# Optimization experiments

Hardware: AMD Instinct MI355X
Metric: run time of the kernel (lower is better)

## Reference

```python
import jax, jax.numpy as jnp
import numpy as np

IN_FEATURES = 8192
OUT_FEATURES = 8192
BATCH = 1024


def setup_inputs() -> dict:
    key = jax.random.key(0)
    kx, kw, kb = jax.random.split(key, 3)
    bound = 1.0 / np.sqrt(IN_FEATURES)  # nn.Linear default init range
    x = jax.random.normal(kx, (BATCH, IN_FEATURES), dtype=jnp.float32)
    W = jax.random.uniform(kw, (OUT_FEATURES, IN_FEATURES), minval=-bound, maxval=bound, dtype=jnp.float32)
    b = jax.random.uniform(kb, (OUT_FEATURES,), minval=-bound, maxval=bound, dtype=jnp.float32)
    return {"x": x, "W": W, "b": b}


def reference(x, W, b):
    # Linear: (B, I) @ (I, O) + (O,) -> (B, O)
    y = jnp.einsum('bi,oi->bo', x, W) + b
    # sum over dim=1, keepdim -> (B, 1)
    y = jnp.sum(y, axis=1, keepdims=True)
    # max over size-1 dim (keepdim) -> identity
    y = jnp.max(y, axis=1, keepdims=True)
    # mean over size-1 dim -> identity
    y = jnp.mean(y, axis=1, keepdims=True)
    # logsumexp over size-1 dim (twice) -> identity
    y = jax.nn.logsumexp(y, axis=1, keepdims=True)
    y = jax.nn.logsumexp(y, axis=1, keepdims=True)
    return y
```

## Files before the change

kernel.cpp:

```cpp
#include <hip/hip_runtime.h>

#define I_FEAT 8192
#define O_FEAT 8192
#define BATCH  1024

#define NS        256
#define ROWS_PB   32
#define CCHUNKS   4
#define SGROUPS   8

using f4 = __attribute__((ext_vector_type(4))) float;

__global__ __launch_bounds__(256) void colsum_partial_kernel(
    const float* __restrict__ W, float* __restrict__ partials) {
  const int chunk = blockIdx.x & (CCHUNKS - 1);
  const int split = blockIdx.x / CCHUNKS;
  const int t = threadIdx.x;
  const int c = (chunk << 11) + (t << 2);

  const float* base = W + (size_t)split * ROWS_PB * I_FEAT + c;

  f4 acc[4][2];
#pragma unroll
  for (int s = 0; s < 4; ++s) { acc[s][0] = (f4)(0.f); acc[s][1] = (f4)(0.f); }

#pragma unroll 8
  for (int r = 0; r < ROWS_PB; ++r) {
    const float* rp = base + (size_t)r * I_FEAT;
    acc[r & 3][0] += *(const f4*)(rp);
    acc[r & 3][1] += *(const f4*)(rp + 1024);
  }

  f4 s0 = (acc[0][0] + acc[1][0]) + (acc[2][0] + acc[3][0]);
  f4 s1 = (acc[0][1] + acc[1][1]) + (acc[2][1] + acc[3][1]);
  float* o = partials + (size_t)split * I_FEAT + c;
  *(f4*)o = s0;
  *(f4*)(o + 1024) = s1;
}

__global__ __launch_bounds__(256) void reduce1_kernel(
    const float* __restrict__ partials, const float* __restrict__ b,
    float* __restrict__ p2, float* __restrict__ bsum) {
  __shared__ float red[4];
  const int t = threadIdx.x;
  if (blockIdx.x < 64) {
    const int cb = blockIdx.x & 7;
    const int sg = blockIdx.x >> 3;
    const int c  = (cb << 10) + (t << 2);
    const float* base = partials + (size_t)sg * (NS / SGROUPS) * I_FEAT + c;
    f4 s = (f4)(0.f);
#pragma unroll 8
    for (int sp = 0; sp < NS / SGROUPS; ++sp)
      s += *(const f4*)(base + (size_t)sp * I_FEAT);
    *(f4*)(p2 + (size_t)sg * I_FEAT + c) = s;
  } else {
    float s = 0.f;
    const f4* b4 = (const f4*)b;
    for (int j = t; j < O_FEAT / 4; j += 256) {
      f4 v = b4[j];
      s += (v.x + v.y) + (v.z + v.w);
    }
#pragma unroll
    for (int off = 32; off; off >>= 1) s += __shfl_down(s, off);
    if ((t & 63) == 0) red[t >> 6] = s;
    __syncthreads();
    if (t == 0) bsum[0] = (red[0] + red[1]) + (red[2] + red[3]);
  }
}

__global__ __launch_bounds__(256) void reduce2_kernel(
    const float* __restrict__ p2, float* __restrict__ colsum) {
  const int c = (blockIdx.x << 10) + (threadIdx.x << 2);
  f4 s = (f4)(0.f);
#pragma unroll
  for (int g = 0; g < SGROUPS; ++g)
    s += *(const f4*)(p2 + (size_t)g * I_FEAT + c);
  *(f4*)(colsum + c) = s;
}

__global__ __launch_bounds__(256) void rowdot_kernel(
    const float* __restrict__ x, const float* __restrict__ colsum,
    const float* __restrict__ bsum, float* __restrict__ out) {
  __shared__ float red[4];
  const int row = blockIdx.x;
  const int t = threadIdx.x;
  const f4* xr = (const f4*)(x + (size_t)row * I_FEAT);
  const f4* cs = (const f4*)colsum;

  float s = 0.f;
#pragma unroll
  for (int j = 0; j < 8; ++j) {
    const int idx = t + j * 256;
    f4 a = xr[idx];
    f4 c = cs[idx];
    s += a.x * c.x + a.y * c.y + a.z * c.z + a.w * c.w;
  }
#pragma unroll
  for (int off = 32; off; off >>= 1) s += __shfl_down(s, off);
  if ((t & 63) == 0) red[t >> 6] = s;
  __syncthreads();
  if (t == 0)
    out[row] = (red[0] + red[1]) + (red[2] + red[3]) + bsum[0];
}

extern "C" void kernel_launch(void* const* d_in, const int* in_sizes, int n_in,
                              void* d_out, int out_size, void* d_ws, size_t ws_size,
                              hipStream_t stream) {
  const float* x = (const float*)d_in[0];
  const float* W = (const float*)d_in[1];
  const float* b = (const float*)d_in[2];
  float* out = (float*)d_out;

  float* partials = (float*)d_ws;
  float* p2       = partials + (size_t)NS * I_FEAT;
  float* colsum   = p2 + (size_t)SGROUPS * I_FEAT;
  float* bsum     = colsum + I_FEAT;

  colsum_partial_kernel<<<NS * CCHUNKS, 256, 0, stream>>>(W, partials);
  reduce1_kernel<<<65, 256, 0, stream>>>(partials, b, p2, bsum);
  reduce2_kernel<<<8, 256, 0, stream>>>(p2, colsum);
  rowdot_kernel<<<BATCH, 256, 0, stream>>>(x, colsum, bsum, out);
}
```

Measured before the change: 61.94 us.

## Restructure column-sum partial kernel to cover full rows with fewer rows per block

```diff
diff --git a/kernel.cpp b/kernel.cpp
--- a/kernel.cpp
+++ b/kernel.cpp
@@ -4,38 +4,35 @@
 #define O_FEAT 8192
 #define BATCH  1024
 
-#define NS        256
-#define ROWS_PB   32
-#define CCHUNKS   4
+#define NS        512
+#define ROWS_PB   16
 #define SGROUPS   8
+#define SPLITS_PER_GROUP (NS / SGROUPS)
 
 using f4 = __attribute__((ext_vector_type(4))) float;
 
 __global__ __launch_bounds__(256) void colsum_partial_kernel(
     const float* __restrict__ W, float* __restrict__ partials) {
-  const int chunk = blockIdx.x & (CCHUNKS - 1);
-  const int split = blockIdx.x / CCHUNKS;
+  const int split = blockIdx.x;
   const int t = threadIdx.x;
-  const int c = (chunk << 11) + (t << 2);
+  const float* base = W + (size_t)split * ROWS_PB * I_FEAT + (t << 2);
 
-  const float* base = W + (size_t)split * ROWS_PB * I_FEAT + c;
+  f4 acc[8];
+#pragma unroll
+  for (int g = 0; g < 8; ++g) acc[g] = (f4)(0.f);
 
-  f4 acc[4][2];
-#pragma unroll
-  for (int s = 0; s < 4; ++s) { acc[s][0] = (f4)(0.f); acc[s][1] = (f4)(0.f); }
-
-#pragma unroll 8
+#pragma unroll 2
   for (int r = 0; r < ROWS_PB; ++r) {
     const float* rp = base + (size_t)r * I_FEAT;
-    acc[r & 3][0] += *(const f4*)(rp);
-    acc[r & 3][1] += *(const f4*)(rp + 1024);
+#pragma unroll
+    for (int g = 0; g < 8; ++g)
+      acc[g] += *(const f4*)(rp + (g << 10));
   }
 
-  f4 s0 = (acc[0][0] + acc[1][0]) + (acc[2][0] + acc[3][0]);
-  f4 s1 = (acc[0][1] + acc[1][1]) + (acc[2][1] + acc[3][1]);
-  float* o = partials + (size_t)split * I_FEAT + c;
-  *(f4*)o = s0;
-  *(f4*)(o + 1024) = s1;
+  float* o = partials + (size_t)split * I_FEAT + (t << 2);
+#pragma unroll
+  for (int g = 0; g < 8; ++g)
+    *(f4*)(o + (g << 10)) = acc[g];
 }
 
 __global__ __launch_bounds__(256) void reduce1_kernel(
@@ -47,10 +44,10 @@
     const int cb = blockIdx.x & 7;
     const int sg = blockIdx.x >> 3;
     const int c  = (cb << 10) + (t << 2);
-    const float* base = partials + (size_t)sg * (NS / SGROUPS) * I_FEAT + c;
+    const float* base = partials + (size_t)sg * SPLITS_PER_GROUP * I_FEAT + c;
     f4 s = (f4)(0.f);
 #pragma unroll 8
-    for (int sp = 0; sp < NS / SGROUPS; ++sp)
+    for (int sp = 0; sp < SPLITS_PER_GROUP; ++sp)
       s += *(const f4*)(base + (size_t)sp * I_FEAT);
     *(f4*)(p2 + (size_t)sg * I_FEAT + c) = s;
   } else {
@@ -116,7 +113,7 @@
   float* colsum   = p2 + (size_t)SGROUPS * I_FEAT;
   float* bsum     = colsum + I_FEAT;
 
-  colsum_partial_kernel<<<NS * CCHUNKS, 256, 0, stream>>>(W, partials);
+  colsum_partial_kernel<<<NS, 256, 0, stream>>>(W, partials);
   reduce1_kernel<<<65, 256, 0, stream>>>(partials, b, p2, bsum);
   reduce2_kernel<<<8, 256, 0, stream>>>(p2, colsum);
   rowdot_kernel<<<BATCH, 256, 0, stream>>>(x, colsum, bsum, out);
```

Result: slower. 67.85 us (+9.5%).
